# Optimization experiments

Measured on AMD Instinct MI355X. Metric: run time of the kernel, lower is better.

Reference implementation:

```python
import jax, jax.numpy as jnp
import numpy as np

NS = (128, 128, 128)       # ns_mesh
NODES = 4                  # interpolation_nodes (P3M, even -> floor-based indexing)
N_POINTS = 100000
N_CHANNELS = 8
BOX = 10.0


def _weights_p3m4(x):
    # x: (P, 3) relative offsets in [-1/2, 1/2]; returns (4, P, 3)
    x2 = x * x
    x3 = x * x2
    c = jnp.asarray(1.0 / 48.0, dtype=x.dtype)
    return jnp.stack([
        c * (1 - 6 * x + 12 * x2 - 8 * x3),
        c * (23 - 30 * x - 12 * x2 + 24 * x3),
        c * (23 + 30 * x - 12 * x2 - 24 * x3),
        c * (1 + 6 * x + 12 * x2 + 8 * x3),
    ])


def setup_inputs() -> dict:
    key = jax.random.key(0)
    k1, k2 = jax.random.split(key)
    positions = jax.random.uniform(k1, (N_POINTS, 3), dtype=jnp.float32) * BOX
    particle_weights = jax.random.normal(k2, (N_POINTS, N_CHANNELS), dtype=jnp.float32)
    cell = jnp.eye(3, dtype=jnp.float32) * BOX
    return {"positions": positions, "particle_weights": particle_weights, "cell": cell}


def reference(positions, particle_weights, cell):
    nx, ny, nz = NS
    ns_f = jnp.array(NS, dtype=positions.dtype)
    inv_cell = jnp.linalg.inv(cell)

    # --- compute_weights ---
    pos_rel = ns_f * (positions @ inv_cell)        # (P,3) mesh-scaled fractional coords
    idx0 = jnp.floor(pos_rel)                      # even nodes -> floor of position
    offsets = pos_rel - (idx0 + 0.5)               # in [-1/2, 1/2]
    w = _weights_p3m4(offsets)                     # (4, P, 3) per-axis 1d weights
    shifts = jnp.arange(1 - (NODES + 1) // 2, 1 + NODES // 2, dtype=jnp.int32)  # [-1,0,1,2]
    ns_i = jnp.array(NS, dtype=jnp.int32)
    idx = (idx0.astype(jnp.int32)[None] + shifts[:, None, None]) % ns_i  # (4,P,3) periodic
    xi, yi, zi = idx[..., 0], idx[..., 1], idx[..., 2]  # (4,P) each

    # 3D outer product of per-axis weights: (4,4,4,P)
    w3 = w[:, None, None, :, 0] * w[None, :, None, :, 1] * w[None, None, :, :, 2]
    # flattened mesh index per (i,j,k,point): (4,4,4,P)
    lin = (xi[:, None, None] * ny + yi[None, :, None]) * nz + zi[None, None, :]

    # --- points_to_mesh: scatter-add weighted charges onto mesh ---
    C = particle_weights.shape[1]
    vals = w3[..., None] * particle_weights        # (4,4,4,P,C)
    rho_flat = jnp.zeros((nx * ny * nz, C), dtype=positions.dtype)
    rho_flat = rho_flat.at[lin.reshape(-1)].add(vals.reshape(-1, C))

    # --- mesh_to_points: gather mesh values back to particle positions ---
    gathered = rho_flat[lin]                       # (4,4,4,P,C)
    out = jnp.sum(gathered * w3[..., None], axis=(0, 1, 2))  # (P,C)
    return out
```

## Files before the change

kernel.cpp:

```cpp
#include <hip/hip_runtime.h>

static constexpr int NXC   = 128;
static constexpr int NPTS  = 100000;
static constexpr int NCH   = 8;
static constexpr int TS    = 8;
static constexpr int NT    = 16;
static constexpr int NTILES = NT * NT * NT;
static constexpr int SLOT  = 64;
static constexpr int REC   = 20;
static constexpr int SLABCAP = 32;
static constexpr int AMAX  = 14 * SLABCAP;
static constexpr int OMAX  = SLOT;
static constexpr int NMAX  = 48;

__device__ __forceinline__ void axis_weights(float x, float w[4]) {
    float x2 = x * x, x3 = x2 * x;
    const float c = 1.0f / 48.0f;
    w[0] = c * (1.0f  - 6.0f  * x + 12.0f * x2 - 8.0f  * x3);
    w[1] = c * (23.0f - 30.0f * x - 12.0f * x2 + 24.0f * x3);
    w[2] = c * (23.0f + 30.0f * x - 12.0f * x2 - 24.0f * x3);
    w[3] = c * (1.0f  + 6.0f  * x + 12.0f * x2 + 8.0f  * x3);
}

__device__ __forceinline__ void mesh_coords(const float* __restrict__ pos,
                                            const float* __restrict__ cell,
                                            int p, float& rx, float& ry, float& rz) {
    float a = cell[0], b = cell[1], c = cell[2];
    float d = cell[3], e = cell[4], f = cell[5];
    float g = cell[6], h = cell[7], i9 = cell[8];
    float c00 = e * i9 - f * h, c01 = f * g - d * i9, c02 = d * h - e * g;
    float c10 = c * h - b * i9, c11 = a * i9 - c * g, c12 = b * g - a * h;
    float c20 = b * f - c * e,  c21 = c * d - a * f,  c22 = a * e - b * d;
    float det = a * c00 + b * c01 + c * c02;
    float s = 128.0f / det;
    float p0 = pos[p * 3 + 0], p1 = pos[p * 3 + 1], p2 = pos[p * 3 + 2];
    rx = s * (p0 * c00 + p1 * c01 + p2 * c02);
    ry = s * (p0 * c10 + p1 * c11 + p2 * c12);
    rz = s * (p0 * c20 + p1 * c21 + p2 * c22);
}

__global__ __launch_bounds__(256) void bin_k(const float* __restrict__ pos,
                                             const float* __restrict__ pw,
                                             const float* __restrict__ cell,
                                             int* __restrict__ cursor,
                                             int* __restrict__ scell,
                                             int* __restrict__ spid,
                                             float* __restrict__ srec) {
    int p = blockIdx.x * 256 + threadIdx.x;
    if (p >= NPTS) return;
    float rx, ry, rz;
    mesh_coords(pos, cell, p, rx, ry, rz);
    float fx = floorf(rx), fy = floorf(ry), fz = floorf(rz);
    int ix = ((int)fx) & (NXC - 1), iy = ((int)fy) & (NXC - 1), iz = ((int)fz) & (NXC - 1);
    int tile = ((ix >> 3) * NT + (iy >> 3)) * NT + (iz >> 3);
    int slot = atomicAdd(cursor + tile, 1);
    if (slot >= SLOT) return;
    int idx = tile * SLOT + slot;
    scell[idx] = ix | (iy << 10) | (iz << 20);
    spid[idx] = p;
    float wx[4], wy[4], wz[4];
    axis_weights(rx - fx - 0.5f, wx);
    axis_weights(ry - fy - 0.5f, wy);
    axis_weights(rz - fz - 0.5f, wz);
    float4* r = reinterpret_cast<float4*>(srec) + (size_t)idx * 5;
    r[0] = make_float4(wx[0], wx[1], wx[2], wx[3]);
    r[1] = make_float4(wy[0], wy[1], wy[2], wy[3]);
    r[2] = make_float4(wz[0], wz[1], wz[2], wz[3]);
    const float4* pw4 = reinterpret_cast<const float4*>(pw + (size_t)p * NCH);
    r[3] = pw4[0];
    r[4] = pw4[1];
}

__device__ __forceinline__ float corr4(float4 wp, float4 wq, int d) {
    float s0 = d == 0 ? wq.x : d == -1 ? wq.y : d == -2 ? wq.z : d == -3 ? wq.w : 0.0f;
    float s1 = d == 1 ? wq.x : d ==  0 ? wq.y : d == -1 ? wq.z : d == -2 ? wq.w : 0.0f;
    float s2 = d == 2 ? wq.x : d ==  1 ? wq.y : d ==  0 ? wq.z : d == -1 ? wq.w : 0.0f;
    float s3 = d == 3 ? wq.x : d ==  2 ? wq.y : d ==  1 ? wq.z : d ==  0 ? wq.w : 0.0f;
    return wp.x * s0 + wp.y * s1 + wp.z * s2 + wp.w * s3;
}

__global__ __launch_bounds__(256) void pair_k(const int* __restrict__ cursor,
                                              const int* __restrict__ scell,
                                              const int* __restrict__ spid,
                                              const float* __restrict__ srec,
                                              float* __restrict__ out) {
    __shared__ int slabA[AMAX];
    __shared__ int slabB[AMAX];
    __shared__ int A1[AMAX];
    __shared__ int A2[AMAX];
    __shared__ int nlist[OMAX * NMAX];
    __shared__ int cnt[OMAX];
    __shared__ int scnt[14];
    __shared__ int soff[15];

    int b = blockIdx.x;
    int tx = b >> 8, ty = (b >> 4) & 15, tz = b & 15;
    int tid = threadIdx.x;
    int lane = tid & 63;
    int nown = min(cursor[b], SLOT);
    if (nown == 0) return;
    int begin = b * SLOT;

    if (tid < 14) scnt[tid] = 0;
    for (int i = tid; i < OMAX; i += 256) cnt[i] = 0;
    __syncthreads();

    int crew = tid >> 3, cl = tid & 7;
    int base_x = tx * TS - 3, base_y = ty * TS - 3, base_z = tz * TS - 3;
    if (crew < 27) {
        int ox = crew / 9 - 1, oy = (crew / 3) % 3 - 1, oz = crew % 3 - 1;
        int nt = ((((tx + ox) & 15) * NT + ((ty + oy) & 15)) * NT) + ((tz + oz) & 15);
        int n0 = nt * SLOT;
        int cn = min(cursor[nt], SLOT);
        for (int s0 = 0; s0 < cn; s0 += 8) {
            int s = s0 + cl;
            if (s < cn) {
                int i = n0 + s;
                int c = scell[i];
                int lcx = ((c & 1023) - base_x) & 127;
                int lcy = (((c >> 10) & 1023) - base_y) & 127;
                int lcz = (((c >> 20) & 1023) - base_z) & 127;
                if (lcx < 14 && lcy < 14 && lcz < 14) {
                    int slot = atomicAdd(&scnt[lcx], 1);
                    if (slot < SLABCAP) {
                        slabA[lcx * SLABCAP + slot] = lcy | (lcz << 5) | (lcx << 10);
                        slabB[lcx * SLABCAP + slot] = i;
                    }
                }
            }
        }
    }
    __syncthreads();
    if (tid == 0) {
        int run = 0;
        #pragma unroll
        for (int s2 = 0; s2 < 14; ++s2) {
            soff[s2] = run;
            run += min(scnt[s2], SLABCAP);
        }
        soff[14] = run;
    }
    __syncthreads();
    for (int u = tid; u < AMAX; u += 256) {
        int s2 = u >> 5, i2 = u & (SLABCAP - 1);
        if (i2 < min(scnt[s2], SLABCAP)) {
            int d = soff[s2] + i2;
            A1[d] = slabA[u];
            A2[d] = slabB[u];
        }
    }
    __syncthreads();

    int sub = tid & 7, pg = tid >> 3;

    for (int p0 = 0; p0 < nown; p0 += 32) {
        int p = p0 + pg;
        bool live = p < nown;
        int lpx = 0, lpyh = 0, lpzh = 0, jbeg = 0, span = 0;
        if (live) {
            int pc = scell[begin + p];
            lpx  = (pc & 1023) - tx * TS;
            lpyh = ((pc >> 10) & 1023) - ty * TS + 3;
            lpzh = ((pc >> 20) & 1023) - tz * TS + 3;
            jbeg = soff[lpx];
            span = soff[lpx + 7] - jbeg;
        }
        int creg = 0;
        for (int j0 = 0; __any(j0 < span); j0 += 8) {
            bool pass = (j0 + sub) < span;
            int a1 = 0, j = jbeg + j0 + sub;
            if (pass) {
                a1 = A1[j];
                int dy3 = (a1 & 31) - lpyh + 3;
                int dz3 = ((a1 >> 5) & 31) - lpzh + 3;
                pass = ((unsigned)dy3 <= 6u) && ((unsigned)dz3 <= 6u);
            }
            unsigned long long m = __ballot(pass);
            int mg = (int)(m >> (lane & 56)) & 255;
            if (pass) {
                int slot = creg + __popc(mg & ((1 << sub) - 1));
                if (slot < NMAX) {
                    int dxp3 = ((a1 >> 10) & 15) - lpx;
                    int dy3 = (a1 & 31) - lpyh + 3;
                    int dz3 = ((a1 >> 5) & 31) - lpzh + 3;
                    int ent = (A2[j] << 9) | (dxp3 << 6) | (dy3 << 3) | dz3;
                    nlist[p * NMAX + slot] = ent;
                }
            }
            creg += __popc(mg);
        }
        if (live && sub == 0) cnt[p] = creg;
    }
    __syncthreads();

    const float4* recs = reinterpret_cast<const float4*>(srec);
    for (int p0 = 0; p0 < nown; p0 += 32) {
        int p = p0 + pg;
        bool live = p < nown;
        int n = 0;
        float4 pxw, pyw, pzw;
        if (live) {
            n = min(cnt[p], NMAX);
            const float4* r = recs + (size_t)(begin + p) * 5;
            pxw = r[0]; pyw = r[1]; pzw = r[2];
        }
        float acc[8] = {0, 0, 0, 0, 0, 0, 0, 0};
        for (int s = sub; s < n; s += 8) {
            int ent = nlist[p * NMAX + s];
            const float4* q = recs + (size_t)(ent >> 9) * 5;
            int dx = ((ent >> 6) & 7) - 3;
            int dy = ((ent >> 3) & 7) - 3;
            int dz = (ent & 7) - 3;
            float4 qxw = q[0], qyw = q[1], qzw = q[2];
            float S = corr4(pxw, qxw, dx) * corr4(pyw, qyw, dy) * corr4(pzw, qzw, dz);
            float4 ch0 = q[3], ch1 = q[4];
            acc[0] += S * ch0.x; acc[1] += S * ch0.y;
            acc[2] += S * ch0.z; acc[3] += S * ch0.w;
            acc[4] += S * ch1.x; acc[5] += S * ch1.y;
            acc[6] += S * ch1.z; acc[7] += S * ch1.w;
        }
        #pragma unroll
        for (int m = 1; m <= 4; m <<= 1) {
            #pragma unroll
            for (int c = 0; c < 8; ++c) acc[c] += __shfl_xor(acc[c], m, 64);
        }
        if (live && sub == 0) {
            int pid = spid[begin + p];
            float4* o = reinterpret_cast<float4*>(out + (size_t)pid * NCH);
            o[0] = make_float4(acc[0], acc[1], acc[2], acc[3]);
            o[1] = make_float4(acc[4], acc[5], acc[6], acc[7]);
        }
    }
}

extern "C" void kernel_launch(void* const* d_in, const int* in_sizes, int n_in,
                              void* d_out, int out_size, void* d_ws, size_t ws_size,
                              hipStream_t stream) {
    const float* pos  = (const float*)d_in[0];
    const float* pw   = (const float*)d_in[1];
    const float* cell = (const float*)d_in[2];
    float* out = (float*)d_out;

    int*   cursor = (int*)d_ws;
    int*   scell  = cursor + NTILES;
    int*   spid   = scell + NTILES * SLOT;
    float* srec   = (float*)(spid + NTILES * SLOT);

    hipMemsetAsync(cursor, 0, NTILES * sizeof(int), stream);

    int pblocks = (NPTS + 255) / 256;
    bin_k<<<pblocks, 256, 0, stream>>>(pos, pw, cell, cursor, scell, spid, srec);
    pair_k<<<NTILES, 256, 0, stream>>>(cursor, scell, spid, srec, out);
}
```

Before: 63.33 us.

## Fuse neighbor-list build with pair accumulation and use transpose-style shuffle reduction

Merges the two per-particle passes (neighbor list construction and pair evaluation) into a single loop so each 8-lane group reuses its own nlist slice, removing the cnt array, one block barrier, and shrinking nlist shared memory. Slab and compacted arrays are packed as int2 to halve LDS accesses. The final 8-channel reduction switches from 24 butterfly shuffles to a recursive-halving scheme (7 shuffles), with each lane writing one channel. Risk: without the barrier between phases, warp-level divergence patterns change, and per-lane scalar stores replace float4 stores.

```diff
diff --git a/kernel.cpp b/kernel.cpp
--- a/kernel.cpp
+++ b/kernel.cpp
@@ -10,8 +10,8 @@
 static constexpr int REC   = 20;
 static constexpr int SLABCAP = 32;
 static constexpr int AMAX  = 14 * SLABCAP;
-static constexpr int OMAX  = SLOT;
 static constexpr int NMAX  = 48;
+static constexpr int NGRP  = 32;
 
 __device__ __forceinline__ void axis_weights(float x, float w[4]) {
     float x2 = x * x, x3 = x2 * x;
@@ -84,12 +84,9 @@
                                               const int* __restrict__ spid,
                                               const float* __restrict__ srec,
                                               float* __restrict__ out) {
-    __shared__ int slabA[AMAX];
-    __shared__ int slabB[AMAX];
-    __shared__ int A1[AMAX];
-    __shared__ int A2[AMAX];
-    __shared__ int nlist[OMAX * NMAX];
-    __shared__ int cnt[OMAX];
+    __shared__ int2 slab[AMAX];
+    __shared__ int2 A12[AMAX];
+    __shared__ int nlist[NGRP * NMAX];
     __shared__ int scnt[14];
     __shared__ int soff[15];
 
@@ -102,7 +99,6 @@
     int begin = b * SLOT;
 
     if (tid < 14) scnt[tid] = 0;
-    for (int i = tid; i < OMAX; i += 256) cnt[i] = 0;
     __syncthreads();
 
     int crew = tid >> 3, cl = tid & 7;
@@ -122,10 +118,9 @@
                 int lcz = (((c >> 20) & 1023) - base_z) & 127;
                 if (lcx < 14 && lcy < 14 && lcz < 14) {
                     int slot = atomicAdd(&scnt[lcx], 1);
-                    if (slot < SLABCAP) {
-                        slabA[lcx * SLABCAP + slot] = lcy | (lcz << 5) | (lcx << 10);
-                        slabB[lcx * SLABCAP + slot] = i;
-                    }
+                    if (slot < SLABCAP)
+                        slab[lcx * SLABCAP + slot] =
+                            make_int2(lcy | (lcz << 5) | (lcx << 10), i);
                 }
             }
         }
@@ -143,20 +138,18 @@
     __syncthreads();
     for (int u = tid; u < AMAX; u += 256) {
         int s2 = u >> 5, i2 = u & (SLABCAP - 1);
-        if (i2 < min(scnt[s2], SLABCAP)) {
-            int d = soff[s2] + i2;
-            A1[d] = slabA[u];
-            A2[d] = slabB[u];
-        }
+        if (i2 < min(scnt[s2], SLABCAP)) A12[soff[s2] + i2] = slab[u];
     }
     __syncthreads();
 
     int sub = tid & 7, pg = tid >> 3;
-
-    for (int p0 = 0; p0 < nown; p0 += 32) {
-        int p = p0 + pg;
+    const float4* recs = reinterpret_cast<const float4*>(srec);
+    int nbl = pg * NMAX;
+
+    for (int p = pg; __any(p < nown); p += NGRP) {
         bool live = p < nown;
-        int lpx = 0, lpyh = 0, lpzh = 0, jbeg = 0, span = 0;
+        int lpx = 0, lpyh = 0, lpzh = 0, jbeg = 0, span = 0, pid = 0;
+        float4 pxw, pyw, pzw;
         if (live) {
             int pc = scell[begin + p];
             lpx  = (pc & 1023) - tx * TS;
@@ -164,13 +157,17 @@
             lpzh = ((pc >> 20) & 1023) - tz * TS + 3;
             jbeg = soff[lpx];
             span = soff[lpx + 7] - jbeg;
+            const float4* r = recs + (size_t)(begin + p) * 5;
+            pxw = r[0]; pyw = r[1]; pzw = r[2];
+            pid = spid[begin + p];
         }
         int creg = 0;
         for (int j0 = 0; __any(j0 < span); j0 += 8) {
             bool pass = (j0 + sub) < span;
-            int a1 = 0, j = jbeg + j0 + sub;
+            int a1 = 0, a2 = 0;
             if (pass) {
-                a1 = A1[j];
+                int2 e = A12[jbeg + j0 + sub];
+                a1 = e.x; a2 = e.y;
                 int dy3 = (a1 & 31) - lpyh + 3;
                 int dz3 = ((a1 >> 5) & 31) - lpzh + 3;
                 pass = ((unsigned)dy3 <= 6u) && ((unsigned)dz3 <= 6u);
@@ -183,30 +180,15 @@
                     int dxp3 = ((a1 >> 10) & 15) - lpx;
                     int dy3 = (a1 & 31) - lpyh + 3;
                     int dz3 = ((a1 >> 5) & 31) - lpzh + 3;
-                    int ent = (A2[j] << 9) | (dxp3 << 6) | (dy3 << 3) | dz3;
-                    nlist[p * NMAX + slot] = ent;
+                    nlist[nbl + slot] = (a2 << 9) | (dxp3 << 6) | (dy3 << 3) | dz3;
                 }
             }
             creg += __popc(mg);
         }
-        if (live && sub == 0) cnt[p] = creg;
-    }
-    __syncthreads();
-
-    const float4* recs = reinterpret_cast<const float4*>(srec);
-    for (int p0 = 0; p0 < nown; p0 += 32) {
-        int p = p0 + pg;
-        bool live = p < nown;
-        int n = 0;
-        float4 pxw, pyw, pzw;
-        if (live) {
-            n = min(cnt[p], NMAX);
-            const float4* r = recs + (size_t)(begin + p) * 5;
-            pxw = r[0]; pyw = r[1]; pzw = r[2];
-        }
+        int n = live ? min(creg, NMAX) : 0;
         float acc[8] = {0, 0, 0, 0, 0, 0, 0, 0};
         for (int s = sub; s < n; s += 8) {
-            int ent = nlist[p * NMAX + s];
+            int ent = nlist[nbl + s];
             const float4* q = recs + (size_t)(ent >> 9) * 5;
             int dx = ((ent >> 6) & 7) - 3;
             int dy = ((ent >> 3) & 7) - 3;
@@ -219,17 +201,24 @@
             acc[4] += S * ch1.x; acc[5] += S * ch1.y;
             acc[6] += S * ch1.z; acc[7] += S * ch1.w;
         }
+        float t4[4];
         #pragma unroll
-        for (int m = 1; m <= 4; m <<= 1) {
-            #pragma unroll
-            for (int c = 0; c < 8; ++c) acc[c] += __shfl_xor(acc[c], m, 64);
-        }
-        if (live && sub == 0) {
-            int pid = spid[begin + p];
-            float4* o = reinterpret_cast<float4*>(out + (size_t)pid * NCH);
-            o[0] = make_float4(acc[0], acc[1], acc[2], acc[3]);
-            o[1] = make_float4(acc[4], acc[5], acc[6], acc[7]);
-        }
+        for (int i = 0; i < 4; ++i) {
+            float keep = (sub & 4) ? acc[i + 4] : acc[i];
+            float send = (sub & 4) ? acc[i]     : acc[i + 4];
+            t4[i] = keep + __shfl_xor(send, 4, 64);
+        }
+        float t2[2];
+        #pragma unroll
+        for (int i = 0; i < 2; ++i) {
+            float keep = (sub & 2) ? t4[i + 2] : t4[i];
+            float send = (sub & 2) ? t4[i]     : t4[i + 2];
+            t2[i] = keep + __shfl_xor(send, 2, 64);
+        }
+        float keep1 = (sub & 1) ? t2[1] : t2[0];
+        float send1 = (sub & 1) ? t2[0] : t2[1];
+        float rres = keep1 + __shfl_xor(send1, 1, 64);
+        if (live) out[(size_t)pid * NCH + sub] = rres;
     }
 }
 
```

New measurement: 61.99 us. 2.1% less time.
